# Kernel optimization log

Measured on AMD Instinct MI355X. Metric: run time of the kernel, lower is better.

The kernel has to match this reference:

```python
import jax, jax.numpy as jnp
import numpy as np

B, LQ, LKV, D, H = 4, 1024, 2048, 1024, 16
HD = D // H
EPS = 1e-5
NEG = -1e9


def _layernorm(x, w, b):
    mu = jnp.mean(x, axis=-1, keepdims=True)
    var = jnp.mean(jnp.square(x - mu), axis=-1, keepdims=True)
    return (x - mu) * jax.lax.rsqrt(var + EPS) * w + b


def setup_inputs() -> dict:
    key = jax.random.key(0)
    ks = jax.random.split(key, 10)
    q = jax.random.normal(ks[0], (B, LQ, D), dtype=jnp.float32)
    kv = jax.random.normal(ks[1], (B, LKV, D), dtype=jnp.float32)
    # ragged kv lengths; mask True == padding
    lengths = jax.random.randint(ks[2], (B,), LKV // 4, LKV + 1)
    mask = jnp.arange(LKV)[None, :] >= lengths[:, None]  # [B, LKV] bool
    s = 1.0 / np.sqrt(D)
    params = dict(
        norm_q_w=jnp.ones((D,), jnp.float32),
        norm_q_b=jnp.zeros((D,), jnp.float32),
        norm_kv_w=jnp.ones((D,), jnp.float32),
        norm_kv_b=jnp.zeros((D,), jnp.float32),
        Wq=jax.random.normal(ks[3], (D, D), jnp.float32) * s,
        bq=jnp.zeros((D,), jnp.float32),
        Wkv=jax.random.normal(ks[4], (2 * D, D), jnp.float32) * s,
        bkv=jnp.zeros((2 * D,), jnp.float32),
        Wo=jax.random.normal(ks[5], (D, D), jnp.float32) * s,
        bo=jnp.zeros((D,), jnp.float32),
    )
    return dict(q=q, kv=kv, mask=mask, **params)


def reference(q, kv, mask, norm_q_w, norm_q_b, norm_kv_w, norm_kv_b, Wq, bq, Wkv, bkv, Wo, bo):
    q_res = q
    qn = _layernorm(q, norm_q_w, norm_q_b)
    kvn = _layernorm(kv, norm_kv_w, norm_kv_b)
    # projections
    qh = (qn @ Wq.T + bq).reshape(B, LQ, H, HD)
    kvp = (kvn @ Wkv.T + bkv).reshape(B, LKV, 2, H, HD)
    k, v = kvp[:, :, 0], kvp[:, :, 1]  # [B, LKV, H, HD]
    # masked cross attention (math-equivalent to varlen flash attn over unpadded kv)
    scale = 1.0 / np.sqrt(HD)
    scores = jnp.einsum('bqhd,bkhd->bhqk', qh, k) * scale
    scores = jnp.where(mask[:, None, None, :], NEG, scores)
    attn = jax.nn.softmax(scores, axis=-1)
    out = jnp.einsum('bhqk,bkhd->bqhd', attn, v).reshape(B, LQ, D)
    # out proj + residual (dropout is identity in eval)
    return q_res + (out @ Wo.T + bo)


if __name__ == '__main__':
    inp = setup_inputs()
    y = reference(**inp)
    print(y.shape, y.dtype)
```

## Files before the change

kernel.cpp:

```cpp
#include <hip/hip_runtime.h>

#define DEV __device__ __forceinline__

typedef unsigned short u16;
typedef float  floatx4 __attribute__((ext_vector_type(4)));
typedef unsigned int uintx4 __attribute__((ext_vector_type(4)));
typedef __bf16 bf16x8 __attribute__((ext_vector_type(8)));

constexpr int cB = 4, cLQ = 1024, cLKV = 2048, cD = 1024, cH = 16, cHD = 64;

DEV u16 f2bf(float f) {
  unsigned u = __builtin_bit_cast(unsigned, f);
  u += 0x7fffu + ((u >> 16) & 1u);
  return (u16)(u >> 16);
}

DEV u16 f2bf_t(float f) {
  return (u16)(__builtin_bit_cast(unsigned, f) >> 16);
}

DEV bf16x8 ld_frag(const u16* p) {
  uintx4 u = *(const uintx4*)p;
  return __builtin_bit_cast(bf16x8, u);
}

DEV floatx4 mfma16(bf16x8 a, bf16x8 b, floatx4 c) {
  return __builtin_amdgcn_mfma_f32_16x16x32_bf16(a, b, c, 0, 0, 0);
}

__global__ __launch_bounds__(256) void prep_kernel(
    const float* __restrict__ q, const float* __restrict__ kv,
    const float* __restrict__ nqw, const float* __restrict__ nqb,
    const float* __restrict__ nkw, const float* __restrict__ nkb,
    u16* __restrict__ qn, u16* __restrict__ kvn,
    const float* __restrict__ Wq, const float* __restrict__ Wkv,
    const float* __restrict__ Wo, u16* __restrict__ wqb,
    u16* __restrict__ wkvb, u16* __restrict__ wob,
    const void* __restrict__ mask, int* __restrict__ lens) {
  int bid = blockIdx.x, tid = threadIdx.x;
  if (bid < cB * (cLQ + cLKV)) {
    const float* x; const float* w; const float* b; u16* dst;
    if (bid < cB * cLQ) {
      x = q + (size_t)bid * cD; w = nqw; b = nqb; dst = qn + (size_t)bid * cD;
    } else {
      int r2 = bid - cB * cLQ;
      x = kv + (size_t)r2 * cD; w = nkw; b = nkb; dst = kvn + (size_t)r2 * cD;
    }
    float4 v = ((const float4*)x)[tid];
    __shared__ float sbuf[8];
    float s = v.x + v.y + v.z + v.w;
    #pragma unroll
    for (int m = 1; m < 64; m <<= 1) s += __shfl_xor(s, m, 64);
    if ((tid & 63) == 0) sbuf[tid >> 6] = s;
    __syncthreads();
    float mean = (sbuf[0] + sbuf[1] + sbuf[2] + sbuf[3]) * (1.f / cD);
    float dx = v.x - mean, dy = v.y - mean, dz = v.z - mean, dw = v.w - mean;
    float ss = dx * dx + dy * dy + dz * dz + dw * dw;
    #pragma unroll
    for (int m = 1; m < 64; m <<= 1) ss += __shfl_xor(ss, m, 64);
    if ((tid & 63) == 0) sbuf[4 + (tid >> 6)] = ss;
    __syncthreads();
    float var = (sbuf[4] + sbuf[5] + sbuf[6] + sbuf[7]) * (1.f / cD);
    float rs = rsqrtf(var + 1e-5f);
    float4 wv = ((const float4*)w)[tid];
    float4 bv = ((const float4*)b)[tid];
    ushort4 o;
    o.x = f2bf(dx * rs * wv.x + bv.x);
    o.y = f2bf(dy * rs * wv.y + bv.y);
    o.z = f2bf(dz * rs * wv.z + bv.z);
    o.w = f2bf(dw * rs * wv.w + bv.w);
    ((ushort4*)dst)[tid] = o;
  } else if (bid < cB * (cLQ + cLKV) + 4096) {
    int gi = (bid - cB * (cLQ + cLKV)) * 256 + tid;
    const float* src; u16* dst; int off;
    if (gi < 262144)      { src = Wq;  dst = wqb;  off = gi; }
    else if (gi < 786432) { src = Wkv; dst = wkvb; off = gi - 262144; }
    else                  { src = Wo;  dst = wob;  off = gi - 786432; }
    float4 v = ((const float4*)src)[off];
    ushort4 o;
    o.x = f2bf(v.x); o.y = f2bf(v.y); o.z = f2bf(v.z); o.w = f2bf(v.w);
    ((ushort4*)dst)[off] = o;
  } else {
    __shared__ int smode;
    __shared__ int cnt[cB];
    if (tid == 0) smode = 0;
    if (tid < cB) cnt[tid] = 0;
    __syncthreads();
    const unsigned* mi = (const unsigned*)mask;
    int bad = 0;
    for (int i = tid; i < cB * cLKV / 4; i += 256)
      if (mi[i] > 1u) bad = 1;
    if (bad) smode = 1;
    __syncthreads();
    if (smode == 0) {
      for (int b = 0; b < cB; b++) {
        int c = 0;
        for (int i = tid; i < cLKV; i += 256) c += (mi[(size_t)b * cLKV + i] == 0u);
        atomicAdd(&cnt[b], c);
      }
    } else {
      const unsigned char* m8 = (const unsigned char*)mask;
      for (int b = 0; b < cB; b++) {
        int c = 0;
        for (int i = tid; i < cLKV; i += 256) c += (m8[(size_t)b * cLKV + i] == 0);
        atomicAdd(&cnt[b], c);
      }
    }
    __syncthreads();
    if (tid < cB) lens[tid] = cnt[tid];
  }
}

struct TileCtx {
  int m16, quad, wr, wc;
};

DEV void gemm_mainloop(const u16* __restrict__ A, const u16* __restrict__ Bm,
                       int row0, int col0, int K, u16* As, u16* Bs,
                       const TileCtx& t, floatx4 (&acc)[4][4]) {
  int tid = threadIdx.x;
  int wave = tid >> 6, lane = tid & 63;
  int srow = wave * 16 + (lane >> 2);
  int sseg = (lane & 3) * 8;
  const u16* ga = A + (size_t)(row0 + srow) * K + sseg;
  const u16* gb = Bm + (size_t)(col0 + srow) * K + sseg;
  const size_t rstep = (size_t)64 * K;
  int woff = srow * 32 + sseg;

  uintx4 a0 = *(const uintx4*)ga;
  uintx4 a1 = *(const uintx4*)(ga + rstep);
  uintx4 b0 = *(const uintx4*)gb;
  uintx4 b1 = *(const uintx4*)(gb + rstep);
  *(uintx4*)(As + woff) = a0;
  *(uintx4*)(As + woff + 2048) = a1;
  *(uintx4*)(Bs + woff) = b0;
  *(uintx4*)(Bs + woff + 2048) = b1;
  a0 = *(const uintx4*)(ga + 32);
  a1 = *(const uintx4*)(ga + rstep + 32);
  b0 = *(const uintx4*)(gb + 32);
  b1 = *(const uintx4*)(gb + rstep + 32);
  __syncthreads();

  for (int k0 = 0; k0 < K; k0 += 32) {
    int cur = (k0 >> 5) & 1;
    const u16* rA = As + cur * 4096;
    const u16* rB = Bs + cur * 4096;
    bf16x8 af[4], bfr[4];
    #pragma unroll
    for (int i = 0; i < 4; i++)
      af[i] = ld_frag(&rA[(t.wr * 64 + i * 16 + t.m16) * 32 + t.quad * 8]);
    #pragma unroll
    for (int j = 0; j < 4; j++)
      bfr[j] = ld_frag(&rB[(t.wc * 64 + j * 16 + t.m16) * 32 + t.quad * 8]);
    if (k0 + 32 < K) {
      u16* nA = As + (cur ^ 1) * 4096 + woff;
      u16* nB = Bs + (cur ^ 1) * 4096 + woff;
      *(uintx4*)nA = a0;
      *(uintx4*)(nA + 2048) = a1;
      *(uintx4*)nB = b0;
      *(uintx4*)(nB + 2048) = b1;
      if (k0 + 64 < K) {
        a0 = *(const uintx4*)(ga + k0 + 64);
        a1 = *(const uintx4*)(ga + rstep + k0 + 64);
        b0 = *(const uintx4*)(gb + k0 + 64);
        b1 = *(const uintx4*)(gb + rstep + k0 + 64);
      }
    }
    #pragma unroll
    for (int i = 0; i < 4; i++)
      #pragma unroll
      for (int j = 0; j < 4; j++)
        acc[i][j] = mfma16(af[i], bfr[j], acc[i][j]);
    __syncthreads();
  }
}

__global__ __launch_bounds__(256) void proj_fused(
    const u16* __restrict__ qn, const u16* __restrict__ wqb,
    const float* __restrict__ bq, u16* __restrict__ qhb,
    const u16* __restrict__ kvn, const u16* __restrict__ wkvb,
    const float* __restrict__ bkv, u16* __restrict__ khb,
    u16* __restrict__ vthb) {
  __shared__ __align__(16) u16 As[2 * 128 * 32];
  __shared__ __align__(16) u16 Bs[2 * 128 * 32];
  int bid = blockIdx.x;
  int lane = threadIdx.x & 63;
  TileCtx t;
  t.m16 = lane & 15; t.quad = lane >> 4;
  int wave = threadIdx.x >> 6;
  t.wr = wave >> 1; t.wc = wave & 1;

  bool isQ = bid < 256;
  int row0, col0;
  const u16* A; const u16* Bm; const float* bias;
  if (isQ) {
    row0 = (bid >> 3) * 128; col0 = (bid & 7) * 128;
    A = qn; Bm = wqb; bias = bq;
  } else {
    int b2 = bid - 256;
    row0 = (b2 >> 4) * 128; col0 = (b2 & 15) * 128;
    A = kvn; Bm = wkvb; bias = bkv;
  }

  floatx4 z = {0.f, 0.f, 0.f, 0.f};
  floatx4 acc[4][4];
  #pragma unroll
  for (int i = 0; i < 4; i++)
    #pragma unroll
    for (int j = 0; j < 4; j++) acc[i][j] = z;

  gemm_mainloop(A, Bm, row0, col0, cD, As, Bs, t, acc);

  #pragma unroll
  for (int j = 0; j < 4; j++) {
    int col = col0 + t.wc * 64 + j * 16 + t.m16;
    float bs = bias[col];
    if (isQ) {
      #pragma unroll
      for (int i = 0; i < 4; i++) {
        int crow = row0 + t.wr * 64 + i * 16 + t.quad * 4;
        #pragma unroll
        for (int r = 0; r < 4; r++)
          qhb[(size_t)(crow + r) * cD + col] = f2bf((acc[i][j][r] + bs) * 0.125f);
      }
    } else {
      bool isK = col < cD;
      int c2 = isK ? col : col - cD;
      int hh = c2 >> 6, dd = c2 & 63;
      #pragma unroll
      for (int i = 0; i < 4; i++) {
        int crow = row0 + t.wr * 64 + i * 16 + t.quad * 4;
        int bb = crow >> 11, kvp = crow & (cLKV - 1);
        if (isK) {
          u16* dst = khb + ((size_t)(bb * cH + hh) * cLKV + kvp) * 64 + dd;
          #pragma unroll
          for (int r = 0; r < 4; r++) dst[(size_t)r * 64] = f2bf(acc[i][j][r] + bs);
        } else {
          u16* dst = vthb + ((size_t)(bb * cH + hh) * 64 + dd) * cLKV + kvp;
          ushort4 o;
          o.x = f2bf(acc[i][j][0] + bs);
          o.y = f2bf(acc[i][j][1] + bs);
          o.z = f2bf(acc[i][j][2] + bs);
          o.w = f2bf(acc[i][j][3] + bs);
          *(ushort4*)dst = o;
        }
      }
    }
  }
}

__global__ __launch_bounds__(256) void gemm_o(
    const u16* __restrict__ A, const u16* __restrict__ Bm,
    const float* __restrict__ bias, const float* __restrict__ res,
    float* __restrict__ Cout, int N, int K) {
  __shared__ __align__(16) u16 As[2 * 128 * 32];
  __shared__ __align__(16) u16 Bs[2 * 128 * 32];
  int lane = threadIdx.x & 63;
  TileCtx t;
  t.m16 = lane & 15; t.quad = lane >> 4;
  int wave = threadIdx.x >> 6;
  t.wr = wave >> 1; t.wc = wave & 1;
  int row0 = blockIdx.y * 128, col0 = blockIdx.x * 128;

  floatx4 z = {0.f, 0.f, 0.f, 0.f};
  floatx4 acc[4][4];
  #pragma unroll
  for (int i = 0; i < 4; i++)
    #pragma unroll
    for (int j = 0; j < 4; j++) acc[i][j] = z;

  gemm_mainloop(A, Bm, row0, col0, K, As, Bs, t, acc);

  #pragma unroll
  for (int j = 0; j < 4; j++) {
    int col = col0 + t.wc * 64 + j * 16 + t.m16;
    float bs = bias[col];
    #pragma unroll
    for (int i = 0; i < 4; i++) {
      int crow = row0 + t.wr * 64 + i * 16 + t.quad * 4;
      #pragma unroll
      for (int r = 0; r < 4; r++) {
        size_t idx = (size_t)(crow + r) * N + col;
        Cout[idx] = acc[i][j][r] + bs + res[idx];
      }
    }
  }
}

constexpr int KS = 72;

template<bool MASK>
DEV void attn_compute(int k0, int len, const u16* __restrict__ Kt,
                      const u16* __restrict__ Vt, u16* __restrict__ psw,
                      bf16x8 aq0, bf16x8 aq1, int m16, int quad,
                      float (&lsum)[4], floatx4 (&accO)[4]) {
  floatx4 z = {0.f, 0.f, 0.f, 0.f};
  floatx4 s[4];
  #pragma unroll
  for (int t = 0; t < 4; t++) {
    bf16x8 bk0 = ld_frag(&Kt[(t * 16 + m16) * KS + quad * 8]);
    bf16x8 bk1 = ld_frag(&Kt[(t * 16 + m16) * KS + 32 + quad * 8]);
    floatx4 tt = z;
    tt = mfma16(aq0, bk0, tt);
    tt = mfma16(aq1, bk1, tt);
    s[t] = tt;
  }
  #pragma unroll
  for (int r = 0; r < 4; r++) {
    float e0, e1, e2, e3;
    if (MASK) {
      int key = k0 + m16;
      e0 = (key < len) ? __expf(s[0][r]) : 0.f;
      e1 = (key + 16 < len) ? __expf(s[1][r]) : 0.f;
      e2 = (key + 32 < len) ? __expf(s[2][r]) : 0.f;
      e3 = (key + 48 < len) ? __expf(s[3][r]) : 0.f;
    } else {
      e0 = __expf(s[0][r]);
      e1 = __expf(s[1][r]);
      e2 = __expf(s[2][r]);
      e3 = __expf(s[3][r]);
    }
    lsum[r] += (e0 + e1) + (e2 + e3);
    int prow = (quad * 4 + r) * KS + m16;
    psw[prow] = f2bf_t(e0);
    psw[prow + 16] = f2bf_t(e1);
    psw[prow + 32] = f2bf_t(e2);
    psw[prow + 48] = f2bf_t(e3);
  }
  bf16x8 ap0 = ld_frag(&psw[m16 * KS + quad * 8]);
  bf16x8 ap1 = ld_frag(&psw[m16 * KS + 32 + quad * 8]);
  #pragma unroll
  for (int db = 0; db < 4; db++) {
    bf16x8 bv0 = ld_frag(&Vt[(db * 16 + m16) * KS + quad * 8]);
    bf16x8 bv1 = ld_frag(&Vt[(db * 16 + m16) * KS + 32 + quad * 8]);
    accO[db] = mfma16(ap0, bv0, accO[db]);
    accO[db] = mfma16(ap1, bv1, accO[db]);
  }
}

__global__ __launch_bounds__(256) void attn_kernel(
    const u16* __restrict__ qh, const u16* __restrict__ kh,
    const u16* __restrict__ vth, const int* __restrict__ lens,
    u16* __restrict__ out) {
  int gid = blockIdx.x;
  int b = gid & (cB - 1);
  int h = (gid >> 2) & (cH - 1);
  int qt = gid >> 6;
  int len = lens[b];
  int wave = threadIdx.x >> 6, lane = threadIdx.x & 63;
  int m16 = lane & 15, quad = lane >> 4;

  __shared__ __align__(16) u16 Kt[64 * KS];
  __shared__ __align__(16) u16 Vt[64 * KS];
  __shared__ __align__(16) u16 Ps[4][16 * KS];
  u16* psw = &Ps[wave][0];

  int qrow = qt * 64 + wave * 16 + m16;
  const u16* qp = qh + ((size_t)(b * cLQ + qrow) * cH + h) * cHD;
  bf16x8 aq0 = ld_frag(qp + quad * 8);
  bf16x8 aq1 = ld_frag(qp + 32 + quad * 8);

  const u16* kbase = kh + (size_t)(b * cH + h) * cLKV * cHD;
  const u16* vbase = vth + (size_t)(b * cH + h) * cHD * cLKV;

  int srow = threadIdx.x >> 3;
  int sseg = threadIdx.x & 7;
  const u16* kg = kbase + (size_t)srow * cHD + sseg * 8;
  const u16* vg = vbase + (size_t)srow * cLKV + sseg * 8;

  float lsum[4] = {0.f, 0.f, 0.f, 0.f};
  floatx4 z = {0.f, 0.f, 0.f, 0.f};
  floatx4 accO[4] = {z, z, z, z};

  int nch = (len + 63) >> 6;
  uintx4 ka  = *(const uintx4*)kg;
  uintx4 kb2 = *(const uintx4*)(kg + (size_t)32 * cHD);
  uintx4 va  = *(const uintx4*)vg;
  uintx4 vb  = *(const uintx4*)(vg + (size_t)32 * cLKV);

  for (int c = 0; c < nch; c++) {
    int k0 = c * 64;
    __syncthreads();
    *(uintx4*)&Kt[srow * KS + sseg * 8] = ka;
    *(uintx4*)&Kt[(srow + 32) * KS + sseg * 8] = kb2;
    *(uintx4*)&Vt[srow * KS + sseg * 8] = va;
    *(uintx4*)&Vt[(srow + 32) * KS + sseg * 8] = vb;
    if (c + 1 < nch) {
      int kn = k0 + 64;
      ka  = *(const uintx4*)(kg + (size_t)kn * cHD);
      kb2 = *(const uintx4*)(kg + (size_t)(kn + 32) * cHD);
      va  = *(const uintx4*)(vg + kn);
      vb  = *(const uintx4*)(vg + (size_t)32 * cLKV + kn);
    }
    __syncthreads();
    if (k0 + 64 <= len)
      attn_compute<false>(k0, len, Kt, Vt, psw, aq0, aq1, m16, quad, lsum, accO);
    else
      attn_compute<true>(k0, len, Kt, Vt, psw, aq0, aq1, m16, quad, lsum, accO);
  }

  #pragma unroll
  for (int r = 0; r < 4; r++) {
    float t = lsum[r];
    #pragma unroll
    for (int m = 1; m < 16; m <<= 1) t += __shfl_xor(t, m, 64);
    lsum[r] = t;
  }

  #pragma unroll
  for (int r = 0; r < 4; r++) {
    float inv = 1.0f / lsum[r];
    int qg = qt * 64 + wave * 16 + quad * 4 + r;
    size_t base = ((size_t)(b * cLQ + qg) * cH + h) * cHD;
    #pragma unroll
    for (int db = 0; db < 4; db++)
      out[base + db * 16 + m16] = f2bf(accO[db][r] * inv);
  }
}

extern "C" void kernel_launch(void* const* d_in, const int* in_sizes, int n_in,
                              void* d_out, int out_size, void* d_ws, size_t ws_size,
                              hipStream_t stream) {
  const float* q    = (const float*)d_in[0];
  const float* kv   = (const float*)d_in[1];
  const void*  mask = d_in[2];
  const float* nqw  = (const float*)d_in[3];
  const float* nqb  = (const float*)d_in[4];
  const float* nkw  = (const float*)d_in[5];
  const float* nkb  = (const float*)d_in[6];
  const float* Wq   = (const float*)d_in[7];
  const float* bq   = (const float*)d_in[8];
  const float* Wkv  = (const float*)d_in[9];
  const float* bkv  = (const float*)d_in[10];
  const float* Wo   = (const float*)d_in[11];
  const float* bo   = (const float*)d_in[12];
  float* out = (float*)d_out;

  char* w = (char*)d_ws;
  int* lens = (int*)w;       w += 256;
  u16* qn   = (u16*)w;       w += (size_t)cB * cLQ * cD * 2;
  u16* kvn  = (u16*)w;       w += (size_t)cB * cLKV * cD * 2;
  u16* wqb  = (u16*)w;       w += (size_t)cD * cD * 2;
  u16* wkvb = (u16*)w;       w += (size_t)2 * cD * cD * 2;
  u16* wob  = (u16*)w;       w += (size_t)cD * cD * 2;
  u16* qhb  = (u16*)w;       w += (size_t)cB * cLQ * cD * 2;
  u16* khb  = (u16*)w;       w += (size_t)cB * cH * cLKV * cHD * 2;
  u16* vthb = (u16*)w;       w += (size_t)cB * cH * cHD * cLKV * 2;
  u16* aob  = (u16*)w;

  prep_kernel<<<cB * (cLQ + cLKV) + 4096 + 1, 256, 0, stream>>>(
      q, kv, nqw, nqb, nkw, nkb, qn, kvn,
      Wq, Wkv, Wo, wqb, wkvb, wob, mask, lens);
  proj_fused<<<1280, 256, 0, stream>>>(
      qn, wqb, bq, qhb, kvn, wkvb, bkv, khb, vthb);
  attn_kernel<<<cB * cH * (cLQ / 64), 256, 0, stream>>>(
      qhb, khb, vthb, lens, aob);
  gemm_o<<<dim3(cD / 128, cB * cLQ / 128), 256, 0, stream>>>(
      aob, wob, bo, q, out, cD, cD);
}
```

Before: 283.9 us.

## Restructure attention: per-wave direct K/V loads, 32 queries per wave, exp2 softmax

The attention kernel stops staging K/V tiles in shared memory with block-wide barriers. Each wave now loads its K and V MFMA fragments straight from global memory, and each wave handles 32 query rows instead of 16 so every fragment is reused twice. The score MFMA operands are swapped, which makes P rows write contiguously to LDS. The Q scale folds in log2(e) so the kernel can use the hardware exp2, and the grid is halved with a remapped block index that groups heads and batches. The cost is more per-wave global/L2 traffic and more registers, and there is still no max subtraction in the softmax, as before.

```diff
diff --git a/kernel.cpp b/kernel.cpp
--- a/kernel.cpp
+++ b/kernel.cpp
@@ -27,6 +27,8 @@
 DEV floatx4 mfma16(bf16x8 a, bf16x8 b, floatx4 c) {
   return __builtin_amdgcn_mfma_f32_16x16x32_bf16(a, b, c, 0, 0, 0);
 }
+
+DEV float ex2(float x) { return __builtin_amdgcn_exp2f(x); }
 
 __global__ __launch_bounds__(256) void prep_kernel(
     const float* __restrict__ q, const float* __restrict__ kv,
@@ -221,7 +223,8 @@
         int crow = row0 + t.wr * 64 + i * 16 + t.quad * 4;
         #pragma unroll
         for (int r = 0; r < 4; r++)
-          qhb[(size_t)(crow + r) * cD + col] = f2bf((acc[i][j][r] + bs) * 0.125f);
+          qhb[(size_t)(crow + r) * cD + col] =
+              f2bf((acc[i][j][r] + bs) * 0.18033688f);
       }
     } else {
       bool isK = col < cD;
@@ -287,54 +290,72 @@
   }
 }
 
-constexpr int KS = 72;
+constexpr int PS = 72;
 
 template<bool MASK>
-DEV void attn_compute(int k0, int len, const u16* __restrict__ Kt,
-                      const u16* __restrict__ Vt, u16* __restrict__ psw,
-                      bf16x8 aq0, bf16x8 aq1, int m16, int quad,
-                      float (&lsum)[4], floatx4 (&accO)[4]) {
+DEV void attn_tile(int k0, int len, const u16* __restrict__ kg,
+                   const u16* __restrict__ vg, u16* __restrict__ psw,
+                   const bf16x8 (&qf)[2][2], int m16, int quad,
+                   float (&lsum)[2], floatx4 (&accO)[2][4]) {
   floatx4 z = {0.f, 0.f, 0.f, 0.f};
-  floatx4 s[4];
+  uintx4 kld[4][2];
   #pragma unroll
   for (int t = 0; t < 4; t++) {
-    bf16x8 bk0 = ld_frag(&Kt[(t * 16 + m16) * KS + quad * 8]);
-    bf16x8 bk1 = ld_frag(&Kt[(t * 16 + m16) * KS + 32 + quad * 8]);
-    floatx4 tt = z;
-    tt = mfma16(aq0, bk0, tt);
-    tt = mfma16(aq1, bk1, tt);
-    s[t] = tt;
-  }
-  #pragma unroll
-  for (int r = 0; r < 4; r++) {
-    float e0, e1, e2, e3;
-    if (MASK) {
-      int key = k0 + m16;
-      e0 = (key < len) ? __expf(s[0][r]) : 0.f;
-      e1 = (key + 16 < len) ? __expf(s[1][r]) : 0.f;
-      e2 = (key + 32 < len) ? __expf(s[2][r]) : 0.f;
-      e3 = (key + 48 < len) ? __expf(s[3][r]) : 0.f;
-    } else {
-      e0 = __expf(s[0][r]);
-      e1 = __expf(s[1][r]);
-      e2 = __expf(s[2][r]);
-      e3 = __expf(s[3][r]);
-    }
-    lsum[r] += (e0 + e1) + (e2 + e3);
-    int prow = (quad * 4 + r) * KS + m16;
-    psw[prow] = f2bf_t(e0);
-    psw[prow + 16] = f2bf_t(e1);
-    psw[prow + 32] = f2bf_t(e2);
-    psw[prow + 48] = f2bf_t(e3);
-  }
-  bf16x8 ap0 = ld_frag(&psw[m16 * KS + quad * 8]);
-  bf16x8 ap1 = ld_frag(&psw[m16 * KS + 32 + quad * 8]);
-  #pragma unroll
-  for (int db = 0; db < 4; db++) {
-    bf16x8 bv0 = ld_frag(&Vt[(db * 16 + m16) * KS + quad * 8]);
-    bf16x8 bv1 = ld_frag(&Vt[(db * 16 + m16) * KS + 32 + quad * 8]);
-    accO[db] = mfma16(ap0, bv0, accO[db]);
-    accO[db] = mfma16(ap1, bv1, accO[db]);
+    const u16* kp = kg + (size_t)(k0 + t * 16) * cHD;
+    kld[t][0] = *(const uintx4*)kp;
+    kld[t][1] = *(const uintx4*)(kp + 32);
+  }
+  uintx4 vld[2][4];
+  #pragma unroll
+  for (int ks = 0; ks < 2; ks++)
+    #pragma unroll
+    for (int db = 0; db < 4; db++)
+      vld[ks][db] = *(const uintx4*)(vg + (size_t)(db * 16) * cLKV + k0 + ks * 32);
+
+  floatx4 s[2][4];
+  #pragma unroll
+  for (int g = 0; g < 2; g++)
+    #pragma unroll
+    for (int t = 0; t < 4; t++) {
+      floatx4 tt = z;
+      tt = mfma16(__builtin_bit_cast(bf16x8, kld[t][0]), qf[g][0], tt);
+      tt = mfma16(__builtin_bit_cast(bf16x8, kld[t][1]), qf[g][1], tt);
+      s[g][t] = tt;
+    }
+
+  #pragma unroll
+  for (int g = 0; g < 2; g++) {
+    #pragma unroll
+    for (int t = 0; t < 4; t++) {
+      float e0, e1, e2, e3;
+      if (MASK) {
+        int key = k0 + t * 16 + quad * 4;
+        e0 = (key     < len) ? ex2(s[g][t][0]) : 0.f;
+        e1 = (key + 1 < len) ? ex2(s[g][t][1]) : 0.f;
+        e2 = (key + 2 < len) ? ex2(s[g][t][2]) : 0.f;
+        e3 = (key + 3 < len) ? ex2(s[g][t][3]) : 0.f;
+      } else {
+        e0 = ex2(s[g][t][0]);
+        e1 = ex2(s[g][t][1]);
+        e2 = ex2(s[g][t][2]);
+        e3 = ex2(s[g][t][3]);
+      }
+      lsum[g] += (e0 + e1) + (e2 + e3);
+      ushort4 pk;
+      pk.x = f2bf_t(e0); pk.y = f2bf_t(e1); pk.z = f2bf_t(e2); pk.w = f2bf_t(e3);
+      *(ushort4*)&psw[(g * 16 + m16) * PS + t * 16 + quad * 4] = pk;
+    }
+  }
+
+  #pragma unroll
+  for (int g = 0; g < 2; g++) {
+    bf16x8 ap0 = ld_frag(&psw[(g * 16 + m16) * PS + quad * 8]);
+    bf16x8 ap1 = ld_frag(&psw[(g * 16 + m16) * PS + 32 + quad * 8]);
+    #pragma unroll
+    for (int db = 0; db < 4; db++) {
+      accO[g][db] = mfma16(ap0, __builtin_bit_cast(bf16x8, vld[0][db]), accO[g][db]);
+      accO[g][db] = mfma16(ap1, __builtin_bit_cast(bf16x8, vld[1][db]), accO[g][db]);
+    }
   }
 }
 
@@ -342,79 +363,55 @@
     const u16* __restrict__ qh, const u16* __restrict__ kh,
     const u16* __restrict__ vth, const int* __restrict__ lens,
     u16* __restrict__ out) {
-  int gid = blockIdx.x;
-  int b = gid & (cB - 1);
-  int h = (gid >> 2) & (cH - 1);
-  int qt = gid >> 6;
+  int bid = blockIdx.x;
+  int i = bid >> 3;
+  int h = (bid & 7) * 2 + (i & 1);
+  int b = ((i >> 1) & 1) | (((i >> 5) & 1) << 1);
+  int qb = (i >> 2) & 7;
   int len = lens[b];
   int wave = threadIdx.x >> 6, lane = threadIdx.x & 63;
   int m16 = lane & 15, quad = lane >> 4;
 
-  __shared__ __align__(16) u16 Kt[64 * KS];
-  __shared__ __align__(16) u16 Vt[64 * KS];
-  __shared__ __align__(16) u16 Ps[4][16 * KS];
+  __shared__ __align__(16) u16 Ps[4][32 * PS];
   u16* psw = &Ps[wave][0];
 
-  int qrow = qt * 64 + wave * 16 + m16;
-  const u16* qp = qh + ((size_t)(b * cLQ + qrow) * cH + h) * cHD;
-  bf16x8 aq0 = ld_frag(qp + quad * 8);
-  bf16x8 aq1 = ld_frag(qp + 32 + quad * 8);
-
-  const u16* kbase = kh + (size_t)(b * cH + h) * cLKV * cHD;
-  const u16* vbase = vth + (size_t)(b * cH + h) * cHD * cLKV;
-
-  int srow = threadIdx.x >> 3;
-  int sseg = threadIdx.x & 7;
-  const u16* kg = kbase + (size_t)srow * cHD + sseg * 8;
-  const u16* vg = vbase + (size_t)srow * cLKV + sseg * 8;
-
-  float lsum[4] = {0.f, 0.f, 0.f, 0.f};
+  int q0 = qb * 128 + wave * 32;
+  const u16* qp = qh + ((size_t)(b * cLQ + q0 + m16) * cH + h) * cHD;
+  bf16x8 qf[2][2];
+  qf[0][0] = ld_frag(qp + quad * 8);
+  qf[0][1] = ld_frag(qp + 32 + quad * 8);
+  qf[1][0] = ld_frag(qp + (size_t)16 * cD + quad * 8);
+  qf[1][1] = ld_frag(qp + (size_t)16 * cD + 32 + quad * 8);
+
+  const u16* kg = kh + (size_t)(b * cH + h) * cLKV * cHD
+                     + (size_t)m16 * cHD + quad * 8;
+  const u16* vg = vth + (size_t)(b * cH + h) * cHD * cLKV
+                      + (size_t)m16 * cLKV + quad * 8;
+
+  float lsum[2] = {0.f, 0.f};
   floatx4 z = {0.f, 0.f, 0.f, 0.f};
-  floatx4 accO[4] = {z, z, z, z};
-
-  int nch = (len + 63) >> 6;
-  uintx4 ka  = *(const uintx4*)kg;
-  uintx4 kb2 = *(const uintx4*)(kg + (size_t)32 * cHD);
-  uintx4 va  = *(const uintx4*)vg;
-  uintx4 vb  = *(const uintx4*)(vg + (size_t)32 * cLKV);
-
-  for (int c = 0; c < nch; c++) {
-    int k0 = c * 64;
-    __syncthreads();
-    *(uintx4*)&Kt[srow * KS + sseg * 8] = ka;
-    *(uintx4*)&Kt[(srow + 32) * KS + sseg * 8] = kb2;
-    *(uintx4*)&Vt[srow * KS + sseg * 8] = va;
-    *(uintx4*)&Vt[(srow + 32) * KS + sseg * 8] = vb;
-    if (c + 1 < nch) {
-      int kn = k0 + 64;
-      ka  = *(const uintx4*)(kg + (size_t)kn * cHD);
-      kb2 = *(const uintx4*)(kg + (size_t)(kn + 32) * cHD);
-      va  = *(const uintx4*)(vg + kn);
-      vb  = *(const uintx4*)(vg + (size_t)32 * cLKV + kn);
-    }
-    __syncthreads();
-    if (k0 + 64 <= len)
-      attn_compute<false>(k0, len, Kt, Vt, psw, aq0, aq1, m16, quad, lsum, accO);
-    else
-      attn_compute<true>(k0, len, Kt, Vt, psw, aq0, aq1, m16, quad, lsum, accO);
-  }
-
-  #pragma unroll
-  for (int r = 0; r < 4; r++) {
-    float t = lsum[r];
-    #pragma unroll
-    for (int m = 1; m < 16; m <<= 1) t += __shfl_xor(t, m, 64);
-    lsum[r] = t;
-  }
-
-  #pragma unroll
-  for (int r = 0; r < 4; r++) {
-    float inv = 1.0f / lsum[r];
-    int qg = qt * 64 + wave * 16 + quad * 4 + r;
-    size_t base = ((size_t)(b * cLQ + qg) * cH + h) * cHD;
-    #pragma unroll
-    for (int db = 0; db < 4; db++)
-      out[base + db * 16 + m16] = f2bf(accO[db][r] * inv);
+  floatx4 accO[2][4] = {{z, z, z, z}, {z, z, z, z}};
+
+  int nfull = len >> 6;
+  for (int c = 0; c < nfull; c++)
+    attn_tile<false>(c * 64, len, kg, vg, psw, qf, m16, quad, lsum, accO);
+  if (len & 63)
+    attn_tile<true>(nfull * 64, len, kg, vg, psw, qf, m16, quad, lsum, accO);
+
+  #pragma unroll
+  for (int g = 0; g < 2; g++) {
+    float tsum = lsum[g];
+    tsum += __shfl_xor(tsum, 16, 64);
+    tsum += __shfl_xor(tsum, 32, 64);
+    #pragma unroll
+    for (int r = 0; r < 4; r++) {
+      float inv = 1.0f / __shfl(tsum, quad * 4 + r, 16);
+      int qg = q0 + g * 16 + quad * 4 + r;
+      size_t base = ((size_t)(b * cLQ + qg) * cH + h) * cHD;
+      #pragma unroll
+      for (int db = 0; db < 4; db++)
+        out[base + db * 16 + m16] = f2bf(accO[g][db][r] * inv);
+    }
   }
 }
 
@@ -453,7 +450,7 @@
       Wq, Wkv, Wo, wqb, wkvb, wob, mask, lens);
   proj_fused<<<1280, 256, 0, stream>>>(
       qn, wqb, bq, qhb, kvn, wkvb, bkv, khb, vthb);
-  attn_kernel<<<cB * cH * (cLQ / 64), 256, 0, stream>>>(
+  attn_kernel<<<512, 256, 0, stream>>>(
       qhb, khb, vthb, lens, aob);
   gemm_o<<<dim3(cD / 128, cB * cLQ / 128), 256, 0, stream>>>(
       aob, wob, bo, q, out, cD, cD);
```

Result: slower. 312.0 us (+9.9%).
